# Optimization experiments

Hardware: AMD Instinct MI355X
Metric: run time of the kernel (lower is better)

The kernel has to match this reference:

```python
import jax, jax.numpy as jnp
import numpy as np

N_MLP = 1024  # number of independent tiny MLPs
D_IN, D_HID, D_OUT = 2, 4, 1
B = 16384


def setup_inputs() -> dict:
    key = jax.random.key(0)
    k = jax.random.split(key, 6)
    x = jax.random.normal(k[0], (B, N_MLP), dtype=jnp.float32)
    x_aug = jax.random.normal(k[1], (B, N_MLP), dtype=jnp.float32)
    # Stacked per-MLP parameters (nn.Linear default init ~ U(-1/sqrt(fan_in), 1/sqrt(fan_in)))
    s1 = 1.0 / np.sqrt(D_IN)
    s2 = 1.0 / np.sqrt(D_HID)
    W1 = jax.random.uniform(k[2], (N_MLP, D_HID, D_IN), jnp.float32, -s1, s1)
    b1 = jax.random.uniform(k[3], (N_MLP, D_HID), jnp.float32, -s1, s1)
    W2 = jax.random.uniform(k[4], (N_MLP, D_OUT, D_HID), jnp.float32, -s2, s2)
    b2 = jax.random.uniform(k[5], (N_MLP, D_OUT), jnp.float32, -s2, s2)
    return {"x": x, "x_aug": x_aug, "W1": W1, "b1": b1, "W2": W2, "b2": b2}


def reference(x, x_aug, W1, b1, W2, b2):
    # data: [B, N, 2] — pair (original, augmented) per feature
    data = jnp.stack([x, x_aug], axis=-1)
    # batched tiny GEMM across the N_MLP axis: [B,N,2] x [N,4,2] -> [B,N,4]
    h = jax.nn.relu(jnp.einsum('bne,nhe->bnh', data, W1) + b1)
    # [B,N,4] x [N,1,4] -> [B,N,1]
    o = jnp.einsum('bnh,noh->bno', h, W2) + b2
    # concat over dim1 of per-MLP [B,1] outputs == squeeze -> [B,N]; mean over N -> [B]
    return jnp.mean(o[..., 0], axis=1)
```

## Files before the change

kernel.cpp:

```cpp
#include <hip/hip_runtime.h>


constexpr int N_MLP = 1024;
constexpr int BATCH = 16384;
constexpr int ROWS = 8;
constexpr int NTHREADS = 256;

__global__ __launch_bounds__(NTHREADS, 4)
void disc_mlp_kernel(const float* __restrict__ x,
                     const float* __restrict__ xa,
                     const float* __restrict__ W1,
                     const float* __restrict__ b1,
                     const float* __restrict__ W2,
                     const float* __restrict__ b2,
                     float* __restrict__ out)
{
    __shared__ float red[ROWS][NTHREADS];

    const int t    = threadIdx.x;
    const int lane = t & 63;
    const int wave = t >> 6;
    const int b0   = blockIdx.x * ROWS;
    const int m0   = t * 4;

    float4 q0[4], q1[4], bv[4], wv[4];
#pragma unroll
    for (int m = 0; m < 4; ++m) {
        q0[m] = reinterpret_cast<const float4*>(W1)[(size_t)(m0 + m) * 2];
        q1[m] = reinterpret_cast<const float4*>(W1)[(size_t)(m0 + m) * 2 + 1];
        bv[m] = reinterpret_cast<const float4*>(b1)[m0 + m];
        wv[m] = reinterpret_cast<const float4*>(W2)[m0 + m];
    }
    const float4 b2v = reinterpret_cast<const float4*>(b2)[t];
    const float bsum = (b2v.x + b2v.y) + (b2v.z + b2v.w);

    const float4* xp = reinterpret_cast<const float4*>(x  + (size_t)b0 * N_MLP) + t;
    const float4* ap = reinterpret_cast<const float4*>(xa + (size_t)b0 * N_MLP) + t;
    constexpr int STRIDE4 = N_MLP / 4;

    float acc[ROWS];
#pragma unroll
    for (int r = 0; r < ROWS; ++r) {
        const float4 xv = xp[r * STRIDE4];
        const float4 av = ap[r * STRIDE4];
        const float xe[4] = {xv.x, xv.y, xv.z, xv.w};
        const float ae[4] = {av.x, av.y, av.z, av.w};
        float s = bsum;
#pragma unroll
        for (int m = 0; m < 4; ++m) {
            float h0 = fmaf(q0[m].x, xe[m], fmaf(q0[m].y, ae[m], bv[m].x));
            float h1 = fmaf(q0[m].z, xe[m], fmaf(q0[m].w, ae[m], bv[m].y));
            float h2 = fmaf(q1[m].x, xe[m], fmaf(q1[m].y, ae[m], bv[m].z));
            float h3 = fmaf(q1[m].z, xe[m], fmaf(q1[m].w, ae[m], bv[m].w));
            h0 = fmaxf(h0, 0.0f);
            h1 = fmaxf(h1, 0.0f);
            h2 = fmaxf(h2, 0.0f);
            h3 = fmaxf(h3, 0.0f);
            s = fmaf(wv[m].x, h0, s);
            s = fmaf(wv[m].y, h1, s);
            s = fmaf(wv[m].z, h2, s);
            s = fmaf(wv[m].w, h3, s);
        }
        acc[r] = s;
    }

#pragma unroll
    for (int r = 0; r < ROWS; ++r) red[r][t] = acc[r];
    __syncthreads();

#pragma unroll
    for (int k = 0; k < ROWS / 4; ++k) {
        const int r = wave * (ROWS / 4) + k;
        float v = (red[r][lane] + red[r][lane + 64]) +
                  (red[r][lane + 128] + red[r][lane + 192]);
        v += __shfl_down(v, 32);
        v += __shfl_down(v, 16);
        v += __shfl_down(v, 8);
        v += __shfl_down(v, 4);
        v += __shfl_down(v, 2);
        v += __shfl_down(v, 1);
        if (lane == 0) out[b0 + r] = v * (1.0f / (float)N_MLP);
    }
}

extern "C" void kernel_launch(void* const* d_in, const int* in_sizes, int n_in,
                              void* d_out, int out_size, void* d_ws, size_t ws_size,
                              hipStream_t stream) {
    const float* x  = (const float*)d_in[0];
    const float* xa = (const float*)d_in[1];
    const float* W1 = (const float*)d_in[2];
    const float* b1 = (const float*)d_in[3];
    const float* W2 = (const float*)d_in[4];
    const float* b2 = (const float*)d_in[5];
    float* out = (float*)d_out;

    disc_mlp_kernel<<<BATCH / ROWS, NTHREADS, 0, stream>>>(x, xa, W1, b1, W2, b2, out);
}
```

Baseline: 157.6 us.

## Pipeline row tiles through LDS with async global_load_lds and persistent blocks

The grid shrinks from 2048 blocks of 8 rows to 1024 persistent blocks that each walk 16 rows. Rows are prefetched four deep into LDS ring buffers with global_load_lds, and progress is gated by manual vmcnt waits and s_barrier. The per-row reduction now uses a wave shuffle plus a small double-buffered LDS cross-wave sum whose final write is delayed by one iteration. The aim is to hide HBM latency with deeper in-flight loads on a bandwidth-bound kernel, at the cost of a barrier per row, fewer blocks, and fragile hand-managed waitcnts.

```diff
diff --git a/kernel.cpp b/kernel.cpp
--- a/kernel.cpp
+++ b/kernel.cpp
@@ -3,8 +3,17 @@
 
 constexpr int N_MLP = 1024;
 constexpr int BATCH = 16384;
-constexpr int ROWS = 8;
 constexpr int NTHREADS = 256;
+constexpr int K = 4;
+constexpr int NBLK = 1024;
+constexpr int TILES = BATCH / NBLK;
+constexpr int PIPE = 4;
+
+typedef __attribute__((address_space(3))) void lds_void;
+typedef const __attribute__((address_space(1))) void gbl_void;
+
+#define WAITVM(N)   asm volatile("s_waitcnt vmcnt(" #N ")" ::: "memory")
+#define WAITLGKM0() asm volatile("s_waitcnt lgkmcnt(0)" ::: "memory")
 
 __global__ __launch_bounds__(NTHREADS, 4)
 void disc_mlp_kernel(const float* __restrict__ x,
@@ -15,13 +24,15 @@
                      const float* __restrict__ b2,
                      float* __restrict__ out)
 {
-    __shared__ float red[ROWS][NTHREADS];
+    __shared__ float xbuf[PIPE][N_MLP];
+    __shared__ float abuf[PIPE][N_MLP];
+    __shared__ float red[2][NTHREADS / 64];
 
     const int t    = threadIdx.x;
     const int lane = t & 63;
     const int wave = t >> 6;
-    const int b0   = blockIdx.x * ROWS;
-    const int m0   = t * 4;
+    const int r0   = blockIdx.x * TILES;
+    const int m0   = t * K;
 
     float4 q0[4], q1[4], bv[4], wv[4];
 #pragma unroll
@@ -34,15 +45,25 @@
     const float4 b2v = reinterpret_cast<const float4*>(b2)[t];
     const float bsum = (b2v.x + b2v.y) + (b2v.z + b2v.w);
 
-    const float4* xp = reinterpret_cast<const float4*>(x  + (size_t)b0 * N_MLP) + t;
-    const float4* ap = reinterpret_cast<const float4*>(xa + (size_t)b0 * N_MLP) + t;
-    constexpr int STRIDE4 = N_MLP / 4;
+    auto stage = [&](int tt) {
+        const int buf = tt & (PIPE - 1);
+        const size_t off = (size_t)(r0 + tt) * N_MLP + wave * 256 + lane * 4;
+        __builtin_amdgcn_global_load_lds((gbl_void*)(x + off),
+            (lds_void*)&xbuf[buf][wave * 256 + lane * 4], 16, 0, 0);
+        __builtin_amdgcn_global_load_lds((gbl_void*)(xa + off),
+            (lds_void*)&abuf[buf][wave * 256 + lane * 4], 16, 0, 0);
+    };
 
-    float acc[ROWS];
-#pragma unroll
-    for (int r = 0; r < ROWS; ++r) {
-        const float4 xv = xp[r * STRIDE4];
-        const float4 av = ap[r * STRIDE4];
+    auto body = [&](int tt) {
+        __builtin_amdgcn_sched_barrier(0);
+        if (tt > 0 && t == ((tt & 3) << 6)) {
+            const int pb = (tt - 1) & 1;
+            float v = (red[pb][0] + red[pb][1]) + (red[pb][2] + red[pb][3]);
+            out[r0 + tt - 1] = v * (1.0f / (float)N_MLP);
+        }
+        const int buf = tt & (PIPE - 1);
+        const float4 xv = reinterpret_cast<const float4*>(xbuf[buf])[t];
+        const float4 av = reinterpret_cast<const float4*>(abuf[buf])[t];
         const float xe[4] = {xv.x, xv.y, xv.z, xv.w};
         const float ae[4] = {av.x, av.y, av.z, av.w};
         float s = bsum;
@@ -52,34 +73,39 @@
             float h1 = fmaf(q0[m].z, xe[m], fmaf(q0[m].w, ae[m], bv[m].y));
             float h2 = fmaf(q1[m].x, xe[m], fmaf(q1[m].y, ae[m], bv[m].z));
             float h3 = fmaf(q1[m].z, xe[m], fmaf(q1[m].w, ae[m], bv[m].w));
-            h0 = fmaxf(h0, 0.0f);
-            h1 = fmaxf(h1, 0.0f);
-            h2 = fmaxf(h2, 0.0f);
-            h3 = fmaxf(h3, 0.0f);
-            s = fmaf(wv[m].x, h0, s);
-            s = fmaf(wv[m].y, h1, s);
-            s = fmaf(wv[m].z, h2, s);
-            s = fmaf(wv[m].w, h3, s);
+            s = fmaf(wv[m].x, fmaxf(h0, 0.0f), s);
+            s = fmaf(wv[m].y, fmaxf(h1, 0.0f), s);
+            s = fmaf(wv[m].z, fmaxf(h2, 0.0f), s);
+            s = fmaf(wv[m].w, fmaxf(h3, 0.0f), s);
         }
-        acc[r] = s;
+        s += __shfl_down(s, 32);
+        s += __shfl_down(s, 16);
+        s += __shfl_down(s, 8);
+        s += __shfl_down(s, 4);
+        s += __shfl_down(s, 2);
+        s += __shfl_down(s, 1);
+        if (lane == 0) red[tt & 1][wave] = s;
+    };
+
+    stage(0); stage(1); stage(2);
+
+    for (int tt = 0; tt < TILES - 3; ++tt) {
+        stage(tt + 3);
+        WAITVM(6);
+        WAITLGKM0();
+        __builtin_amdgcn_s_barrier();
+        body(tt);
     }
+    WAITVM(4); WAITLGKM0(); __builtin_amdgcn_s_barrier(); body(TILES - 3);
+    WAITVM(2); WAITLGKM0(); __builtin_amdgcn_s_barrier(); body(TILES - 2);
+    WAITVM(0); WAITLGKM0(); __builtin_amdgcn_s_barrier(); body(TILES - 1);
 
-#pragma unroll
-    for (int r = 0; r < ROWS; ++r) red[r][t] = acc[r];
-    __syncthreads();
-
-#pragma unroll
-    for (int k = 0; k < ROWS / 4; ++k) {
-        const int r = wave * (ROWS / 4) + k;
-        float v = (red[r][lane] + red[r][lane + 64]) +
-                  (red[r][lane + 128] + red[r][lane + 192]);
-        v += __shfl_down(v, 32);
-        v += __shfl_down(v, 16);
-        v += __shfl_down(v, 8);
-        v += __shfl_down(v, 4);
-        v += __shfl_down(v, 2);
-        v += __shfl_down(v, 1);
-        if (lane == 0) out[b0 + r] = v * (1.0f / (float)N_MLP);
+    WAITLGKM0();
+    __builtin_amdgcn_s_barrier();
+    if (t == ((TILES & 3) << 6)) {
+        const int pb = (TILES - 1) & 1;
+        float v = (red[pb][0] + red[pb][1]) + (red[pb][2] + red[pb][3]);
+        out[r0 + TILES - 1] = v * (1.0f / (float)N_MLP);
     }
 }
 
@@ -94,5 +120,5 @@
     const float* b2 = (const float*)d_in[5];
     float* out = (float*)d_out;
 
-    disc_mlp_kernel<<<BATCH / ROWS, NTHREADS, 0, stream>>>(x, xa, W1, b1, W2, b2, out);
+    disc_mlp_kernel<<<NBLK, NTHREADS, 0, stream>>>(x, xa, W1, b1, W2, b2, out);
 }
```

Measured after the change: 157.4 us. About the same (-0.1%).

## Split MLP axis across blocks, stage inputs via global_load_lds, reduce with atomics

Applied to the files above, without the earlier changes.

Splits the 1024-MLP axis into four quarter blocks, quadrupling the grid so each block handles 8 rows by 256 MLPs. Inputs are copied into LDS with global_load_lds instead of register loads. The cross-wave LDS reduction and its barrier are replaced by a wave shuffle reduction plus float atomicAdd into the output. This adds a separate zeroing kernel launch, loads 4x more weights per output row, and makes the summation order nondeterministic.

```diff
diff --git a/kernel.cpp b/kernel.cpp
--- a/kernel.cpp
+++ b/kernel.cpp
@@ -5,6 +5,17 @@
 constexpr int BATCH = 16384;
 constexpr int ROWS = 8;
 constexpr int NTHREADS = 256;
+constexpr int QN = 256;
+constexpr int NQ = N_MLP / QN;
+constexpr int NBLK = (BATCH / ROWS) * NQ;
+
+typedef __attribute__((address_space(3))) void lds_void;
+typedef const __attribute__((address_space(1))) void gbl_void;
+
+__global__ __launch_bounds__(256)
+void zero_out_kernel(float* __restrict__ out) {
+    out[blockIdx.x * 256 + threadIdx.x] = 0.0f;
+}
 
 __global__ __launch_bounds__(NTHREADS, 4)
 void disc_mlp_kernel(const float* __restrict__ x,
@@ -15,71 +26,69 @@
                      const float* __restrict__ b2,
                      float* __restrict__ out)
 {
-    __shared__ float red[ROWS][NTHREADS];
+    __shared__ float xbuf[ROWS * QN];
+    __shared__ float abuf[ROWS * QN];
 
     const int t    = threadIdx.x;
     const int lane = t & 63;
     const int wave = t >> 6;
-    const int b0   = blockIdx.x * ROWS;
-    const int m0   = t * 4;
+    const int q    = blockIdx.x & (NQ - 1);
+    const int rb   = blockIdx.x >> 2;
+    const int b0   = rb * ROWS;
+    const int n0   = q * QN + lane * 4;
 
-    float4 q0[4], q1[4], bv[4], wv[4];
+    const float* gx = x  + q * QN;
+    const float* ga = xa + q * QN;
+#pragma unroll
+    for (int i = 0; i < 2; ++i) {
+        const int r = wave * 2 + i;
+        const size_t off = (size_t)(b0 + r) * N_MLP + lane * 4;
+        __builtin_amdgcn_global_load_lds((gbl_void*)(gx + off),
+            (lds_void*)&xbuf[r * QN + lane * 4], 16, 0, 0);
+        __builtin_amdgcn_global_load_lds((gbl_void*)(ga + off),
+            (lds_void*)&abuf[r * QN + lane * 4], 16, 0, 0);
+    }
+
+    float4 wa[4], wb[4], bv[4], wv[4];
 #pragma unroll
     for (int m = 0; m < 4; ++m) {
-        q0[m] = reinterpret_cast<const float4*>(W1)[(size_t)(m0 + m) * 2];
-        q1[m] = reinterpret_cast<const float4*>(W1)[(size_t)(m0 + m) * 2 + 1];
-        bv[m] = reinterpret_cast<const float4*>(b1)[m0 + m];
-        wv[m] = reinterpret_cast<const float4*>(W2)[m0 + m];
+        wa[m] = reinterpret_cast<const float4*>(W1)[(size_t)(n0 + m) * 2];
+        wb[m] = reinterpret_cast<const float4*>(W1)[(size_t)(n0 + m) * 2 + 1];
+        bv[m] = reinterpret_cast<const float4*>(b1)[n0 + m];
+        wv[m] = reinterpret_cast<const float4*>(W2)[n0 + m];
     }
-    const float4 b2v = reinterpret_cast<const float4*>(b2)[t];
+    const float4 b2v = reinterpret_cast<const float4*>(b2)[n0 >> 2];
     const float bsum = (b2v.x + b2v.y) + (b2v.z + b2v.w);
 
-    const float4* xp = reinterpret_cast<const float4*>(x  + (size_t)b0 * N_MLP) + t;
-    const float4* ap = reinterpret_cast<const float4*>(xa + (size_t)b0 * N_MLP) + t;
-    constexpr int STRIDE4 = N_MLP / 4;
+    asm volatile("s_waitcnt vmcnt(0)" ::: "memory");
 
-    float acc[ROWS];
 #pragma unroll
-    for (int r = 0; r < ROWS; ++r) {
-        const float4 xv = xp[r * STRIDE4];
-        const float4 av = ap[r * STRIDE4];
+    for (int i = 0; i < 2; ++i) {
+        const int r = wave * 2 + i;
+        const float4 xv = reinterpret_cast<const float4*>(xbuf)[r * (QN / 4) + lane];
+        const float4 av = reinterpret_cast<const float4*>(abuf)[r * (QN / 4) + lane];
         const float xe[4] = {xv.x, xv.y, xv.z, xv.w};
         const float ae[4] = {av.x, av.y, av.z, av.w};
         float s = bsum;
 #pragma unroll
         for (int m = 0; m < 4; ++m) {
-            float h0 = fmaf(q0[m].x, xe[m], fmaf(q0[m].y, ae[m], bv[m].x));
-            float h1 = fmaf(q0[m].z, xe[m], fmaf(q0[m].w, ae[m], bv[m].y));
-            float h2 = fmaf(q1[m].x, xe[m], fmaf(q1[m].y, ae[m], bv[m].z));
-            float h3 = fmaf(q1[m].z, xe[m], fmaf(q1[m].w, ae[m], bv[m].w));
-            h0 = fmaxf(h0, 0.0f);
-            h1 = fmaxf(h1, 0.0f);
-            h2 = fmaxf(h2, 0.0f);
-            h3 = fmaxf(h3, 0.0f);
-            s = fmaf(wv[m].x, h0, s);
-            s = fmaf(wv[m].y, h1, s);
-            s = fmaf(wv[m].z, h2, s);
-            s = fmaf(wv[m].w, h3, s);
+            float h0 = fmaf(wa[m].x, xe[m], fmaf(wa[m].y, ae[m], bv[m].x));
+            float h1 = fmaf(wa[m].z, xe[m], fmaf(wa[m].w, ae[m], bv[m].y));
+            float h2 = fmaf(wb[m].x, xe[m], fmaf(wb[m].y, ae[m], bv[m].z));
+            float h3 = fmaf(wb[m].z, xe[m], fmaf(wb[m].w, ae[m], bv[m].w));
+            s = fmaf(wv[m].x, fmaxf(h0, 0.0f), s);
+            s = fmaf(wv[m].y, fmaxf(h1, 0.0f), s);
+            s = fmaf(wv[m].z, fmaxf(h2, 0.0f), s);
+            s = fmaf(wv[m].w, fmaxf(h3, 0.0f), s);
         }
-        acc[r] = s;
-    }
-
-#pragma unroll
-    for (int r = 0; r < ROWS; ++r) red[r][t] = acc[r];
-    __syncthreads();
-
-#pragma unroll
-    for (int k = 0; k < ROWS / 4; ++k) {
-        const int r = wave * (ROWS / 4) + k;
-        float v = (red[r][lane] + red[r][lane + 64]) +
-                  (red[r][lane + 128] + red[r][lane + 192]);
-        v += __shfl_down(v, 32);
-        v += __shfl_down(v, 16);
-        v += __shfl_down(v, 8);
-        v += __shfl_down(v, 4);
-        v += __shfl_down(v, 2);
-        v += __shfl_down(v, 1);
-        if (lane == 0) out[b0 + r] = v * (1.0f / (float)N_MLP);
+        s += __shfl_down(s, 32);
+        s += __shfl_down(s, 16);
+        s += __shfl_down(s, 8);
+        s += __shfl_down(s, 4);
+        s += __shfl_down(s, 2);
+        s += __shfl_down(s, 1);
+        if (lane == 0)
+            atomicAdd(out + b0 + r, s * (1.0f / (float)N_MLP));
     }
 }
 
@@ -94,5 +103,6 @@
     const float* b2 = (const float*)d_in[5];
     float* out = (float*)d_out;
 
-    disc_mlp_kernel<<<BATCH / ROWS, NTHREADS, 0, stream>>>(x, xa, W1, b1, W2, b2, out);
+    zero_out_kernel<<<BATCH / 256, 256, 0, stream>>>(out);
+    disc_mlp_kernel<<<NBLK, NTHREADS, 0, stream>>>(x, xa, W1, b1, W2, b2, out);
 }
```

Measured after the change: 175.8 us. +11.6%, slower.
